# Kernel optimization log

Hardware: AMD Instinct MI355X
Metric: run time of the kernel (lower is better)

## Reference

```python
import jax, jax.numpy as jnp
import numpy as np

B, T, I, U, BB = 256, 1024, 64, 128, 256


def lecun_tanh(x):
    return 1.7159 * jnp.tanh(0.666 * x)


def _linear_init(key, fan_in, fan_out):
    # torch nn.Linear default: U(-1/sqrt(fan_in), 1/sqrt(fan_in)) for weight and bias
    kw, kb = jax.random.split(key)
    lim = 1.0 / np.sqrt(fan_in)
    W = jax.random.uniform(kw, (fan_in, fan_out), jnp.float32, -lim, lim)
    b = jax.random.uniform(kb, (fan_out,), jnp.float32, -lim, lim)
    return W, b


def setup_inputs() -> dict:
    key = jax.random.key(0)
    ks = jax.random.split(key, 6)
    x = jax.random.normal(ks[0], (B, T, I), jnp.float32)
    W_bb, b_bb = _linear_init(ks[1], I + U, BB)
    W_ff1, b_ff1 = _linear_init(ks[2], BB, U)
    W_ff2, b_ff2 = _linear_init(ks[3], BB, U)
    W_ta, b_ta = _linear_init(ks[4], BB, U)
    W_tb, b_tb = _linear_init(ks[5], BB, U)
    return {
        "x": x,
        "W_bb": W_bb, "b_bb": b_bb,
        "W_ff1": W_ff1, "b_ff1": b_ff1,
        "W_ff2": W_ff2, "b_ff2": b_ff2,
        "W_ta": W_ta, "b_ta": b_ta,
        "W_tb": W_tb, "b_tb": b_tb,
    }


def reference(x, W_bb, b_bb, W_ff1, b_ff1, W_ff2, b_ff2, W_ta, b_ta, W_tb, b_tb):
    # CfC, non-wired, mode='default', activation='lecun_tanh', backbone_layers=1,
    # mixed_memory=False, proj_size=None (fc = Identity), timespans=None (ts = 1.0).
    ts = jnp.float32(1.0)

    def step(h, xt):
        z = jnp.concatenate([xt, h], axis=-1)            # [B, I+U]
        z = lecun_tanh(z @ W_bb + b_bb)                   # backbone, [B, BB]
        ff1 = jnp.tanh(z @ W_ff1 + b_ff1)                 # [B, U]
        ff2 = jnp.tanh(z @ W_ff2 + b_ff2)                 # [B, U]
        t_a = z @ W_ta + b_ta
        t_b = z @ W_tb + b_tb
        t_interp = jax.nn.sigmoid(t_a * ts + t_b)
        h_new = ff1 * (1.0 - t_interp) + t_interp * ff2
        return h_new, h_new

    h0 = jnp.zeros((x.shape[0], W_ff1.shape[1]), x.dtype)
    h_last, ys = jax.lax.scan(step, h0, jnp.swapaxes(x, 0, 1))  # scan over T
    readout = jnp.swapaxes(ys, 0, 1)                      # [B, T, U]
    return readout, h_last
```

## Files before the change

### kernel.cpp

```cpp
#include <hip/hip_runtime.h>


typedef __bf16 bf16;
typedef __bf16 bf16x8 __attribute__((ext_vector_type(8)));
typedef float  f32x4  __attribute__((ext_vector_type(4)));

#define BDIM 512

constexpr int B_  = 256;
constexpr int T_  = 1024;
constexpr int I_  = 64;
constexpr int U_  = 128;
constexpr int BB_ = 256;
constexpr int ROWS = 16;
constexpr int NBLK = B_ / ROWS;
constexpr int KO1  = (I_ + U_) / 8;

__device__ __forceinline__ float tanh_fast(float x) {
  float e = __builtin_amdgcn_exp2f(x * 2.8853900817779268f);
  return 1.0f - 2.0f * __builtin_amdgcn_rcpf(e + 1.0f);
}
__device__ __forceinline__ float sigmoid_fast(float x) {
  return __builtin_amdgcn_rcpf(1.0f + __builtin_amdgcn_exp2f(x * -1.4426950408889634f));
}

__device__ __forceinline__ void barrier_lds() {
  asm volatile("s_waitcnt lgkmcnt(0)" ::: "memory");
  __builtin_amdgcn_s_barrier();
}

__global__ __launch_bounds__(BDIM, 2)
void cfc_kernel(const float* __restrict__ x,
                const float* __restrict__ Wbb,  const float* __restrict__ bbb,
                const float* __restrict__ Wff1, const float* __restrict__ bff1,
                const float* __restrict__ Wff2, const float* __restrict__ bff2,
                const float* __restrict__ Wta,  const float* __restrict__ bta,
                const float* __restrict__ Wtb,  const float* __restrict__ btb,
                float* __restrict__ out)
{
  __shared__ __align__(16) bf16 Abuf[KO1 * ROWS * 8];
  __shared__ __align__(16) bf16 Zbuf[32  * ROWS * 8];

  const int tid  = threadIdx.x;
  const int w    = tid >> 6;
  const int l    = tid & 63;
  const int quad = l >> 4;
  const int l16  = l & 15;
  const int bg   = blockIdx.x;

  const int c1 = w * 32 + l16;
  const int u  = w * 16 + l16;

  bf16x8 f1[6][2];
  #pragma unroll
  for (int ks = 0; ks < 6; ks++)
    #pragma unroll
    for (int nt = 0; nt < 2; nt++)
      #pragma unroll
      for (int j = 0; j < 8; j++) {
        int k = ks * 32 + quad * 8 + j;
        f1[ks][nt][j] = (bf16)Wbb[k * BB_ + c1 + nt * 16];
      }

  bf16x8 g2[8][3];
  #pragma unroll
  for (int r = 0; r < 8; r++) {
    int ks = (w + r) & 7;
    #pragma unroll
    for (int j = 0; j < 8; j++) {
      int k = ks * 32 + quad * 8 + j;
      g2[r][0][j] = (bf16)Wff1[k * U_ + u];
      g2[r][1][j] = (bf16)Wff2[k * U_ + u];
      g2[r][2][j] = (bf16)(Wta[k * U_ + u] + Wtb[k * U_ + u]);
    }
  }

  const float bz0 = bbb[c1];
  const float bz1 = bbb[c1 + 16];
  const float bh0 = bff1[u];
  const float bh1 = bff2[u];
  const float bh2 = bta[u] + btb[u];

  for (int idx = tid; idx < (KO1 - 8) * ROWS * 8; idx += BDIM)
    Abuf[8 * ROWS * 8 + idx] = (bf16)0.0f;

  const int xm  = tid >> 5;
  const int xkk = tid & 31;
  const float* xsrc = x + ((size_t)(bg * ROWS + xm) * T_) * I_ + 2 * xkk;
  bf16* xdst = &Abuf[(((2 * xkk) >> 3) * ROWS + xm) * 8 + ((2 * xkk) & 7)];

  {
    float2 v = *(const float2*)xsrc;
    xdst[0] = (bf16)v.x;
    xdst[1] = (bf16)v.y;
  }
  __syncthreads();

  float* outp  = out + (size_t)(bg * ROWS) * T_ * U_ + u;
  float* hlast = out + (size_t)B_ * T_ * U_ + (size_t)(bg * ROWS) * U_ + u;

  const int h_oct = (64 + u) >> 3;
  const int h_sub = (64 + u) & 7;

  float hreg[4];

  for (int t = 0; t < T_; ++t) {
    const int tn = (t + 1 < T_) ? (t + 1) : (T_ - 1);
    float2 xv = *(const float2*)(xsrc + (size_t)tn * I_);

    f32x4 az0 = { bz0, bz0, bz0, bz0 };
    f32x4 az1 = { bz1, bz1, bz1, bz1 };
    #pragma unroll
    for (int ks = 0; ks < 6; ks++) {
      bf16x8 a = *(const bf16x8*)&Abuf[((ks * 4 + quad) * ROWS + l16) * 8];
      az0 = __builtin_amdgcn_mfma_f32_16x16x32_bf16(a, f1[ks][0], az0, 0, 0, 0);
      az1 = __builtin_amdgcn_mfma_f32_16x16x32_bf16(a, f1[ks][1], az1, 0, 0, 0);
    }
    #pragma unroll
    for (int i = 0; i < 4; i++) {
      int m = quad * 4 + i;
      float z0 = 1.7159f * tanh_fast(0.666f * az0[i]);
      float z1 = 1.7159f * tanh_fast(0.666f * az1[i]);
      int c0 = c1, cB = c1 + 16;
      Zbuf[((c0 >> 3) * ROWS + m) * 8 + (c0 & 7)] = (bf16)z0;
      Zbuf[((cB >> 3) * ROWS + m) * 8 + (cB & 7)] = (bf16)z1;
    }

    f32x4 a0 = { bh0, bh0, bh0, bh0 };
    f32x4 a1 = { bh1, bh1, bh1, bh1 };
    f32x4 a2 = { bh2, bh2, bh2, bh2 };
    {
      bf16x8 zf = *(const bf16x8*)&Zbuf[((w * 4 + quad) * ROWS + l16) * 8];
      a0 = __builtin_amdgcn_mfma_f32_16x16x32_bf16(zf, g2[0][0], a0, 0, 0, 0);
      a1 = __builtin_amdgcn_mfma_f32_16x16x32_bf16(zf, g2[0][1], a1, 0, 0, 0);
      a2 = __builtin_amdgcn_mfma_f32_16x16x32_bf16(zf, g2[0][2], a2, 0, 0, 0);
    }
    barrier_lds();

    #pragma unroll
    for (int r = 1; r < 8; r++) {
      int ks = (w + r) & 7;
      bf16x8 zf = *(const bf16x8*)&Zbuf[((ks * 4 + quad) * ROWS + l16) * 8];
      a0 = __builtin_amdgcn_mfma_f32_16x16x32_bf16(zf, g2[r][0], a0, 0, 0, 0);
      a1 = __builtin_amdgcn_mfma_f32_16x16x32_bf16(zf, g2[r][1], a1, 0, 0, 0);
      a2 = __builtin_amdgcn_mfma_f32_16x16x32_bf16(zf, g2[r][2], a2, 0, 0, 0);
    }

    #pragma unroll
    for (int i = 0; i < 4; i++) {
      int m = quad * 4 + i;
      float ff1 = tanh_fast(a0[i]);
      float ff2 = tanh_fast(a1[i]);
      float s   = sigmoid_fast(a2[i]);
      float h   = ff1 + s * (ff2 - ff1);
      hreg[i]   = h;
      outp[(size_t)m * T_ * U_ + (size_t)t * U_] = h;
      Abuf[(h_oct * ROWS + m) * 8 + h_sub] = (bf16)h;
    }

    xdst[0] = (bf16)xv.x;
    xdst[1] = (bf16)xv.y;

    barrier_lds();
  }

  #pragma unroll
  for (int i = 0; i < 4; i++)
    hlast[(size_t)(quad * 4 + i) * U_] = hreg[i];
}

extern "C" void kernel_launch(void* const* d_in, const int* in_sizes, int n_in,
                              void* d_out, int out_size, void* d_ws, size_t ws_size,
                              hipStream_t stream) {
  const float* x    = (const float*)d_in[0];
  const float* Wbb  = (const float*)d_in[1];
  const float* bbb  = (const float*)d_in[2];
  const float* Wff1 = (const float*)d_in[3];
  const float* bff1 = (const float*)d_in[4];
  const float* Wff2 = (const float*)d_in[5];
  const float* bff2 = (const float*)d_in[6];
  const float* Wta  = (const float*)d_in[7];
  const float* bta  = (const float*)d_in[8];
  const float* Wtb  = (const float*)d_in[9];
  const float* btb  = (const float*)d_in[10];
  float* out = (float*)d_out;
  (void)in_sizes; (void)n_in; (void)out_size; (void)d_ws; (void)ws_size;

  hipLaunchKernelGGL(cfc_kernel, dim3(NBLK), dim3(BDIM), 0, stream,
                     x, Wbb, bbb, Wff1, bff1, Wff2, bff2, Wta, bta, Wtb, btb, out);
}
```

Baseline: 1.595 ms.

## Precompute input projection in a parallel prepass, shorten recurrent backbone matmul

Adds a separate prepass kernel that computes x·W_bb[:64]+b_bb in fp32 for all timesteps into the workspace. The recurrent kernel then seeds the backbone accumulator from this buffer and runs only 4 MFMA k-steps over h instead of 6, which shortens the serial per-step critical path. The third MFMA chain is also split so the tanh of ff1/ff2 can overlap with the gate accumulation. The cost is a 256 MB intermediate written and then read back, plus an extra launch. The original kernel is kept as a fallback for when the workspace is too small.

Result: slower. 1.944 ms (+21.9%).

```diff
diff --git a/kernel.cpp b/kernel.cpp
--- a/kernel.cpp
+++ b/kernel.cpp
@@ -23,14 +23,194 @@
 __device__ __forceinline__ float sigmoid_fast(float x) {
   return __builtin_amdgcn_rcpf(1.0f + __builtin_amdgcn_exp2f(x * -1.4426950408889634f));
 }
-
 __device__ __forceinline__ void barrier_lds() {
   asm volatile("s_waitcnt lgkmcnt(0)" ::: "memory");
   __builtin_amdgcn_s_barrier();
 }
 
+__global__ __launch_bounds__(256)
+void cfc_prepass(const float* __restrict__ x, const float* __restrict__ Wbb,
+                 const float* __restrict__ bbb, float* __restrict__ px)
+{
+  __shared__ float xs[16][64];
+  const int g  = blockIdx.x;
+  const int bg = g >> 10, t = g & 1023;
+  const int tid = threadIdx.x;
+
+  {
+    const int r = tid >> 4, k4 = (tid & 15) * 4;
+    float4 v = *(const float4*)(x + ((size_t)(bg * ROWS + r) * T_ + t) * I_ + k4);
+    *(float4*)&xs[r][k4] = v;
+  }
+
+  float wcol[64];
+  #pragma unroll
+  for (int k = 0; k < 64; k++) wcol[k] = Wbb[k * BB_ + tid];
+
+  float acc[16];
+  const float bb = bbb[tid];
+  #pragma unroll
+  for (int r = 0; r < 16; r++) acc[r] = bb;
+
+  __syncthreads();
+
+  #pragma unroll
+  for (int k4 = 0; k4 < 16; k4++) {
+    #pragma unroll
+    for (int r = 0; r < 16; r++) {
+      float4 xq = *(const float4*)&xs[r][k4 * 4];
+      acc[r] += xq.x * wcol[k4 * 4]     + xq.y * wcol[k4 * 4 + 1]
+              + xq.z * wcol[k4 * 4 + 2] + xq.w * wcol[k4 * 4 + 3];
+    }
+  }
+
+  float* dst = px + ((size_t)g * BB_ + tid) * ROWS;
+  #pragma unroll
+  for (int r4 = 0; r4 < 4; r4++) {
+    float4 v = { acc[r4 * 4], acc[r4 * 4 + 1], acc[r4 * 4 + 2], acc[r4 * 4 + 3] };
+    *(float4*)(dst + r4 * 4) = v;
+  }
+}
+
 __global__ __launch_bounds__(BDIM, 2)
-void cfc_kernel(const float* __restrict__ x,
+void cfc_main_px(const float* __restrict__ px,
+                 const float* __restrict__ Wbb,
+                 const float* __restrict__ Wff1, const float* __restrict__ bff1,
+                 const float* __restrict__ Wff2, const float* __restrict__ bff2,
+                 const float* __restrict__ Wta,  const float* __restrict__ bta,
+                 const float* __restrict__ Wtb,  const float* __restrict__ btb,
+                 float* __restrict__ out)
+{
+  __shared__ __align__(16) bf16 Abuf[16 * ROWS * 8];
+  __shared__ __align__(16) bf16 Zbuf[32 * ROWS * 8];
+
+  const int tid  = threadIdx.x;
+  const int w    = tid >> 6;
+  const int l    = tid & 63;
+  const int quad = l >> 4;
+  const int l16  = l & 15;
+  const int bg   = blockIdx.x;
+
+  const int c1 = w * 32 + l16;
+  const int u  = w * 16 + l16;
+
+  bf16x8 f1[4][2];
+  #pragma unroll
+  for (int ks = 0; ks < 4; ks++)
+    #pragma unroll
+    for (int nt = 0; nt < 2; nt++)
+      #pragma unroll
+      for (int j = 0; j < 8; j++) {
+        int k = 64 + ks * 32 + quad * 8 + j;
+        f1[ks][nt][j] = (bf16)Wbb[k * BB_ + c1 + nt * 16];
+      }
+
+  bf16x8 g2[8][3];
+  #pragma unroll
+  for (int r = 0; r < 8; r++) {
+    int ks = (w + r) & 7;
+    #pragma unroll
+    for (int j = 0; j < 8; j++) {
+      int k = ks * 32 + quad * 8 + j;
+      g2[r][0][j] = (bf16)Wff1[k * U_ + u];
+      g2[r][1][j] = (bf16)Wff2[k * U_ + u];
+      g2[r][2][j] = (bf16)(Wta[k * U_ + u] + Wtb[k * U_ + u]);
+    }
+  }
+
+  const float bh0 = bff1[u];
+  const float bh1 = bff2[u];
+  const float bh2 = bta[u] + btb[u];
+
+  for (int idx = tid; idx < 16 * ROWS * 8; idx += BDIM) Abuf[idx] = (bf16)0.0f;
+
+  const float* pxb = px + (size_t)bg * T_ * BB_ * ROWS / 16 * 16;
+  const size_t o0 = (size_t)c1 * ROWS + quad * 4;
+  const size_t o1 = (size_t)(c1 + 16) * ROWS + quad * 4;
+
+  float4 pxv0 = *(const float4*)(pxb + o0);
+  float4 pxv1 = *(const float4*)(pxb + o1);
+
+  __syncthreads();
+
+  float* outp  = out + (size_t)(bg * ROWS) * T_ * U_ + u;
+  float* hlast = out + (size_t)B_ * T_ * U_ + (size_t)(bg * ROWS) * U_ + u;
+
+  const int h_oct = u >> 3, h_sub = u & 7;
+  float hreg[4];
+
+  for (int t = 0; t < T_; ++t) {
+    const int tn = (t + 1 < T_) ? (t + 1) : (T_ - 1);
+    float4 nx0 = *(const float4*)(pxb + (size_t)tn * BB_ * ROWS + o0);
+    float4 nx1 = *(const float4*)(pxb + (size_t)tn * BB_ * ROWS + o1);
+
+    f32x4 az0 = { pxv0.x, pxv0.y, pxv0.z, pxv0.w };
+    f32x4 az1 = { pxv1.x, pxv1.y, pxv1.z, pxv1.w };
+    #pragma unroll
+    for (int ks = 0; ks < 4; ks++) {
+      bf16x8 a = *(const bf16x8*)&Abuf[((ks * 4 + quad) * ROWS + l16) * 8];
+      az0 = __builtin_amdgcn_mfma_f32_16x16x32_bf16(a, f1[ks][0], az0, 0, 0, 0);
+      az1 = __builtin_amdgcn_mfma_f32_16x16x32_bf16(a, f1[ks][1], az1, 0, 0, 0);
+    }
+    #pragma unroll
+    for (int i = 0; i < 4; i++) {
+      int m = quad * 4 + i;
+      float z0 = 1.7159f * tanh_fast(0.666f * az0[i]);
+      float z1 = 1.7159f * tanh_fast(0.666f * az1[i]);
+      Zbuf[((c1 >> 3) * ROWS + m) * 8 + (c1 & 7)] = (bf16)z0;
+      Zbuf[(((c1 + 16) >> 3) * ROWS + m) * 8 + ((c1 + 16) & 7)] = (bf16)z1;
+    }
+
+    f32x4 a0 = { bh0, bh0, bh0, bh0 };
+    f32x4 a1 = { bh1, bh1, bh1, bh1 };
+    f32x4 a2 = { bh2, bh2, bh2, bh2 };
+    {
+      bf16x8 zf = *(const bf16x8*)&Zbuf[((w * 4 + quad) * ROWS + l16) * 8];
+      a0 = __builtin_amdgcn_mfma_f32_16x16x32_bf16(zf, g2[0][0], a0, 0, 0, 0);
+      a1 = __builtin_amdgcn_mfma_f32_16x16x32_bf16(zf, g2[0][1], a1, 0, 0, 0);
+      a2 = __builtin_amdgcn_mfma_f32_16x16x32_bf16(zf, g2[0][2], a2, 0, 0, 0);
+    }
+    barrier_lds();
+
+    #pragma unroll
+    for (int r = 1; r < 8; r++) {
+      int ks = (w + r) & 7;
+      bf16x8 zf = *(const bf16x8*)&Zbuf[((ks * 4 + quad) * ROWS + l16) * 8];
+      a0 = __builtin_amdgcn_mfma_f32_16x16x32_bf16(zf, g2[r][0], a0, 0, 0, 0);
+      a1 = __builtin_amdgcn_mfma_f32_16x16x32_bf16(zf, g2[r][1], a1, 0, 0, 0);
+    }
+    float ff1[4], ff2[4];
+    #pragma unroll
+    for (int r = 1; r < 8; r++) {
+      int ks = (w + r) & 7;
+      bf16x8 zf = *(const bf16x8*)&Zbuf[((ks * 4 + quad) * ROWS + l16) * 8];
+      a2 = __builtin_amdgcn_mfma_f32_16x16x32_bf16(zf, g2[r][2], a2, 0, 0, 0);
+      if (r <= 4) {
+        ff1[r - 1] = tanh_fast(a0[r - 1]);
+        ff2[r - 1] = tanh_fast(a1[r - 1]);
+      }
+    }
+
+    #pragma unroll
+    for (int i = 0; i < 4; i++) {
+      int m = quad * 4 + i;
+      float s = sigmoid_fast(a2[i]);
+      float h = ff1[i] + s * (ff2[i] - ff1[i]);
+      hreg[i] = h;
+      outp[(size_t)m * T_ * U_ + (size_t)t * U_] = h;
+      Abuf[(h_oct * ROWS + m) * 8 + h_sub] = (bf16)h;
+    }
+    pxv0 = nx0; pxv1 = nx1;
+    barrier_lds();
+  }
+
+  #pragma unroll
+  for (int i = 0; i < 4; i++)
+    hlast[(size_t)(quad * 4 + i) * U_] = hreg[i];
+}
+
+__global__ __launch_bounds__(BDIM, 2)
+void cfc_kernel_noPx(const float* __restrict__ x,
                 const float* __restrict__ Wbb,  const float* __restrict__ bbb,
                 const float* __restrict__ Wff1, const float* __restrict__ bff1,
                 const float* __restrict__ Wff2, const float* __restrict__ bff2,
@@ -101,7 +281,6 @@
 
   const int h_oct = (64 + u) >> 3;
   const int h_sub = (64 + u) & 7;
-
   float hreg[4];
 
   for (int t = 0; t < T_; ++t) {
@@ -121,9 +300,8 @@
       int m = quad * 4 + i;
       float z0 = 1.7159f * tanh_fast(0.666f * az0[i]);
       float z1 = 1.7159f * tanh_fast(0.666f * az1[i]);
-      int c0 = c1, cB = c1 + 16;
-      Zbuf[((c0 >> 3) * ROWS + m) * 8 + (c0 & 7)] = (bf16)z0;
-      Zbuf[((cB >> 3) * ROWS + m) * 8 + (cB & 7)] = (bf16)z1;
+      Zbuf[((c1 >> 3) * ROWS + m) * 8 + (c1 & 7)] = (bf16)z0;
+      Zbuf[(((c1 + 16) >> 3) * ROWS + m) * 8 + ((c1 + 16) & 7)] = (bf16)z1;
     }
 
     f32x4 a0 = { bh0, bh0, bh0, bh0 };
@@ -184,8 +362,17 @@
   const float* Wtb  = (const float*)d_in[9];
   const float* btb  = (const float*)d_in[10];
   float* out = (float*)d_out;
-  (void)in_sizes; (void)n_in; (void)out_size; (void)d_ws; (void)ws_size;
-
-  hipLaunchKernelGGL(cfc_kernel, dim3(NBLK), dim3(BDIM), 0, stream,
-                     x, Wbb, bbb, Wff1, bff1, Wff2, bff2, Wta, bta, Wtb, btb, out);
-}
+  (void)in_sizes; (void)n_in; (void)out_size;
+
+  const size_t px_bytes = (size_t)B_ * T_ * BB_ * sizeof(float);
+  if (ws_size >= px_bytes) {
+    float* px = (float*)d_ws;
+    hipLaunchKernelGGL(cfc_prepass, dim3(NBLK * T_), dim3(256), 0, stream,
+                       x, Wbb, bbb, px);
+    hipLaunchKernelGGL(cfc_main_px, dim3(NBLK), dim3(BDIM), 0, stream,
+                       px, Wbb, Wff1, bff1, Wff2, bff2, Wta, bta, Wtb, btb, out);
+  } else {
+    hipLaunchKernelGGL(cfc_kernel_noPx, dim3(NBLK), dim3(BDIM), 0, stream,
+                       x, Wbb, bbb, Wff1, bff1, Wff2, bff2, Wta, bta, Wtb, btb, out);
+  }
+}
```
